# Kernel tuning notes

Measured on AMD Instinct MI355X. Metric: run time of the kernel, lower is better.

The kernel has to match this reference:

```python
import jax, jax.numpy as jnp
import numpy as np

B, NF, L, DEPTH = 128, 1781, 2048, 4
DI, DS, DC, DTR = 8, 32, 4, 1  # d_inner=expand*d_model, d_state, d_conv, dt_rank


def setup_inputs() -> dict:
    key = jax.random.key(0)
    ks = jax.random.split(key, 32)
    n = lambda k, s, sc=0.02: jax.random.normal(k, s, jnp.float32) * sc
    inp = {
        'x': jax.random.normal(ks[0], (B, NF), jnp.float32),
        # projection1: ReLU -> Linear(NF,2048) -> LayerNorm(2048)
        'p1_W': n(ks[1], (L, NF)), 'p1_b': jnp.zeros((L,), jnp.float32),
        'ln1_g': jnp.ones((L,), jnp.float32), 'ln1_b': jnp.zeros((L,), jnp.float32),
        # per-block Mamba params stacked over depth
        'in_W': n(ks[2], (DEPTH, 2 * DI, 1)),
        'conv_w': n(ks[3], (DEPTH, DI, 1, DC), 0.2),
        'conv_b': jnp.zeros((DEPTH, DI), jnp.float32),
        'xp_W': n(ks[4], (DEPTH, DTR + 2 * DS, DI)),
        'dt_W': n(ks[5], (DEPTH, DI, DTR), 0.5),
        'dt_b': n(ks[6], (DEPTH, DI), 0.5) - 4.0,
        'A_log': jnp.log(jnp.tile(jnp.arange(1, DS + 1, dtype=jnp.float32), (DEPTH, DI, 1))),
        'Dp': jnp.ones((DEPTH, DI), jnp.float32),
        'out_W': n(ks[7], (DEPTH, 1, DI)),
        'rms_w': jnp.ones((DEPTH, 1), jnp.float32),
        # projection2: Linear(2048,512) -> LayerNorm(512) -> ReLU -> Linear(512,256)
        'p2a_W': n(ks[8], (512, L)), 'p2a_b': jnp.zeros((512,), jnp.float32),
        'ln2_g': jnp.ones((512,), jnp.float32), 'ln2_b': jnp.zeros((512,), jnp.float32),
        'p2b_W': n(ks[9], (256, 512)), 'p2b_b': jnp.zeros((256,), jnp.float32),
    }
    return inp


def _layernorm(x, g, b, eps=1e-5):
    m = x.mean(-1, keepdims=True)
    v = ((x - m) ** 2).mean(-1, keepdims=True)
    return (x - m) * jax.lax.rsqrt(v + eps) * g + b


def _silu(x):
    return x * jax.nn.sigmoid(x)


def _mamba(x, in_W, conv_w, conv_b, xp_W, dt_W, dt_b, A_log, Dp, out_W):
    # x: (B, L, 1)
    xz = x @ in_W.T                      # (B, L, 2*DI)
    xc, z = jnp.split(xz, 2, axis=-1)    # (B, L, DI) each
    # causal depthwise conv over L
    xt = jnp.transpose(xc, (0, 2, 1))    # (B, DI, L)
    xt = jax.lax.conv_general_dilated(xt, conv_w, (1,), [(DC - 1, 0)],
                                      dimension_numbers=('NCH', 'OIH', 'NCH'),
                                      feature_group_count=DI)
    xc = _silu(jnp.transpose(xt, (0, 2, 1)) + conv_b)   # (B, L, DI)
    x_dbl = xc @ xp_W.T                                  # (B, L, DTR+2*DS)
    dt, Bm, Cm = jnp.split(x_dbl, [DTR, DTR + DS], axis=-1)
    dt = jax.nn.softplus(dt @ dt_W.T + dt_b)             # (B, L, DI)
    A = -jnp.exp(A_log)                                  # (DI, DS)
    dA = jnp.exp(dt[..., None] * A)                      # (B, L, DI, DS)
    dBx = dt[..., None] * Bm[:, :, None, :] * xc[..., None]
    def comb(e1, e2):
        a1, b1 = e1
        a2, b2 = e2
        return (a2 * a1, a2 * b1 + b2)
    _, h = jax.lax.associative_scan(comb, (dA, dBx), axis=1)  # h: (B,L,DI,DS)
    y = jnp.einsum('blds,bls->bld', h, Cm) + Dp * xc
    y = y * _silu(z)
    return y @ out_W.T                                   # (B, L, 1)


def reference(x, p1_W, p1_b, ln1_g, ln1_b, in_W, conv_w, conv_b, xp_W, dt_W, dt_b,
              A_log, Dp, out_W, rms_w, p2a_W, p2a_b, ln2_g, ln2_b, p2b_W, p2b_b):
    h = jax.nn.relu(x) @ p1_W.T + p1_b
    h = _layernorm(h, ln1_g, ln1_b)
    h = h[..., None]                      # (B, L, 1)
    for i in range(DEPTH):
        # RMSNorm over last dim (size 1): mean(x^2) == x^2
        rn = h * jax.lax.rsqrt(h * h + 1e-5) * rms_w[i]
        h = _mamba(rn, in_W[i], conv_w[i], conv_b[i], xp_W[i], dt_W[i], dt_b[i],
                   A_log[i], Dp[i], out_W[i]) + h
    h = h[..., 0]
    h2 = h @ p2a_W.T + p2a_b
    h2 = jax.nn.relu(_layernorm(h2, ln2_g, ln2_b))
    return h2 @ p2b_W.T + p2b_b
```

## Files before the change

### kernel.cpp

```cpp
#include <hip/hip_runtime.h>
#include <math.h>

#define B_    128
#define NF_   1781
#define L_    2048
#define DEPTH_ 4
#define DI_   8
#define DS_   32
#define NXD_  65
#define NC_   32
#define CL_   64
#define MCL_  64
#define KS1_  8
#define KS3_  8
#define LOG2E_ 1.44269504088896f

__device__ __forceinline__ float silu_f(float x) {
    return x / (1.f + __expf(-x));
}
__device__ __forceinline__ float softplus_f(float x) {
    return fmaxf(x, 0.f) + __logf(1.f + __expf(-fabsf(x)));
}
__device__ __forceinline__ float exp2_fast(float x) {
#if __has_builtin(__builtin_amdgcn_exp2f)
    return __builtin_amdgcn_exp2f(x);
#else
    return __expf(x * 0.6931471805599453f);
#endif
}

#define DPP_ADD(x, ctrl)                                                      \
    (x) += __int_as_float(__builtin_amdgcn_update_dpp(                        \
        0, __float_as_int(x), (ctrl), 0xf, 0xf, true))

__device__ __forceinline__ float dpp_sum32_tail(float x) {
    DPP_ADD(x, 0x111);
    DPP_ADD(x, 0x112);
    DPP_ADD(x, 0x114);
    DPP_ADD(x, 0x118);
    DPP_ADD(x, 0x142);
    return x;
}

__device__ __forceinline__ float wave_sum64(float v) {
    v += __shfl_xor(v, 32); v += __shfl_xor(v, 16); v += __shfl_xor(v, 8);
    v += __shfl_xor(v, 4);  v += __shfl_xor(v, 2);  v += __shfl_xor(v, 1);
    return v;
}

__device__ __forceinline__ float block_sum256(float v, float* red) {
    v = wave_sum64(v);
    int tid = threadIdx.x;
    __syncthreads();
    if ((tid & 63) == 0) red[tid >> 6] = v;
    __syncthreads();
    return red[0] + red[1] + red[2] + red[3];
}

__global__ __launch_bounds__(256) void kZero(float4* __restrict__ p) {
    p[blockIdx.x * 256 + threadIdx.x] = make_float4(0.f, 0.f, 0.f, 0.f);
}

__global__ __launch_bounds__(256) void k1_gemm(const float* __restrict__ x,
                                               const float* __restrict__ W,
                                               float* __restrict__ g1) {
    __shared__ float As[32][20];
    __shared__ float Bs[32][65];
    const int n0 = blockIdx.x * 64, m0 = blockIdx.y * 16;
    const int kb = blockIdx.z * 224;
    const int tid = threadIdx.x;
    const int tn = tid & 63, tm = tid >> 6;
    float acc[4] = {0.f, 0.f, 0.f, 0.f};
#pragma unroll 1
    for (int t = 0; t < 7; ++t) {
        const int k0 = kb + t * 32;
#pragma unroll
        for (int j = 0; j < 2; ++j) {
            int idx = tid + 256 * j, k = idx & 31, m = idx >> 5;
            int kk = k0 + k;
            float v = (kk < NF_) ? x[(m0 + m) * NF_ + kk] : 0.f;
            As[k][m] = fmaxf(v, 0.f);
        }
#pragma unroll
        for (int j = 0; j < 8; ++j) {
            int idx = tid + 256 * j, k = idx & 31, n = idx >> 5;
            int kk = k0 + k;
            Bs[k][n] = (kk < NF_) ? W[(size_t)(n0 + n) * NF_ + kk] : 0.f;
        }
        __syncthreads();
#pragma unroll
        for (int k = 0; k < 32; ++k) {
            float4 a = *(const float4*)&As[k][tm * 4];
            float b0 = Bs[k][tn];
            acc[0] = fmaf(a.x, b0, acc[0]);
            acc[1] = fmaf(a.y, b0, acc[1]);
            acc[2] = fmaf(a.z, b0, acc[2]);
            acc[3] = fmaf(a.w, b0, acc[3]);
        }
        __syncthreads();
    }
#pragma unroll
    for (int r = 0; r < 4; ++r)
        atomicAdd(&g1[(m0 + tm * 4 + r) * L_ + n0 + tn], acc[r]);
}

__global__ __launch_bounds__(256) void kLN(float* __restrict__ hg,
                                           const float* __restrict__ bias,
                                           const float* __restrict__ g,
                                           const float* __restrict__ bt) {
    __shared__ float red[4];
    const int tid = threadIdx.x;
    float* h = hg + blockIdx.x * L_;
    float s = 0.f;
    for (int l = tid; l < L_; l += 256) s += h[l] + bias[l];
    s = block_sum256(s, red);
    const float mean = s * (1.f / (float)L_);
    float vs = 0.f;
    for (int l = tid; l < L_; l += 256) {
        float d = h[l] + bias[l] - mean; vs += d * d;
    }
    vs = block_sum256(vs, red);
    const float rstd = rsqrtf(vs * (1.f / (float)L_) + 1e-5f);
    for (int l = tid; l < L_; l += 256)
        h[l] = (h[l] + bias[l] - mean) * rstd * g[l] + bt[l];
}

#define PHASE_LOAD(NEED_ALL)                                                   \
    {                                                                          \
        const float rmsw = rms_w[dep];                                         \
        if (tid < CL_ + 3) {                                                   \
            int lg = c0 - 3 + tid;                                             \
            float hv = (lg >= 0) ? hg[(size_t)b * L_ + lg] : 0.f;              \
            rnb[tid] = (lg >= 0) ? hv * rsqrtf(hv * hv + 1e-5f) * rmsw : 0.f;  \
        }                                                                      \
        int t2 = tid - (CL_ + 3);                                              \
        if (t2 >= 0 && t2 < 32)       Pp[t2]      = conv_w[dep * 32 + t2];     \
        else if (t2 >= 32 && t2 < 40) Pp[t2]      = conv_b[dep * 8 + t2 - 32]; \
        else if (t2 >= 40 && t2 < 56) Pp[t2]      = in_W[dep * 16 + t2 - 40];  \
        else if (t2 >= 56 && t2 < 64) Pp[t2]      = dt_W[dep * 8 + t2 - 56];   \
        else if (t2 >= 64 && t2 < 72) Pp[t2]      = dt_b[dep * 8 + t2 - 64];   \
        else if (NEED_ALL && t2 >= 72 && t2 < 80) Pp[t2] = Dp[dep * 8 + t2 - 72]; \
        else if (NEED_ALL && t2 >= 80 && t2 < 88) Pp[t2] = out_W[dep * 8 + t2 - 80]; \
    }                                                                          \
    __syncthreads();

#define PHASE_CONV()                                                           \
    {                                                                          \
        const int dd = tid & 7, lb = tid >> 3;                                 \
        const float cw0 = Pp[dd * 4], cw1 = Pp[dd * 4 + 1];                    \
        const float cw2 = Pp[dd * 4 + 2], cw3 = Pp[dd * 4 + 3];                \
        const float inw = Pp[40 + dd], cb = Pp[32 + dd];                       \
        const float xp0d = xp_W[dep * (NXD_ * 8) + dd];                        \
        _Pragma("unroll")                                                      \
        for (int jj = 0; jj < CL_ / 32; ++jj) {                                \
            int l = lb + 32 * jj;                                              \
            float sc = cw0 * rnb[l] + cw1 * rnb[l + 1] +                       \
                       cw2 * rnb[l + 2] + cw3 * rnb[l + 3];                    \
            float v = silu_f(inw * sc + cb);                                   \
            xcvb[l * 12 + dd] = v;                                             \
            float p = v * xp0d;                                                \
            DPP_ADD(p, 0x111); DPP_ADD(p, 0x112); DPP_ADD(p, 0x114);          \
            if (dd == 7) dtrawS[l] = p;                                        \
        }                                                                      \
    }                                                                          \
    __syncthreads();

#define PHASE_DT()                                                             \
    {                                                                          \
        const int dd = tid & 7, lb = tid >> 3;                                 \
        const float dtw = Pp[56 + dd], dtb = Pp[64 + dd];                      \
        _Pragma("unroll")                                                      \
        for (int jj = 0; jj < CL_ / 32; ++jj) {                                \
            int l = lb + 32 * jj;                                              \
            float dt = softplus_f(dtrawS[l] * dtw + dtb);                      \
            dtuS[l * 8 + dd] = make_float2(dt * LOG2E_,                        \
                                           dt * xcvb[l * 12 + dd]);            \
        }                                                                      \
    }

__global__ __launch_bounds__(256) void kA(int dep,
    const float* __restrict__ hg, float2* __restrict__ PS,
    const float* __restrict__ in_W,  const float* __restrict__ conv_w,
    const float* __restrict__ conv_b,const float* __restrict__ xp_W,
    const float* __restrict__ dt_W,  const float* __restrict__ dt_b,
    const float* __restrict__ A_log, const float* __restrict__ Dp,
    const float* __restrict__ out_W, const float* __restrict__ rms_w) {
    __shared__ float rnb[CL_ + 3];
    __shared__ float Pp[88];
    __shared__ float xcvb[CL_ * 12];
    __shared__ float dtrawS[CL_];
    __shared__ float BmS[CL_ * 32];
    __shared__ float2 dtuS[CL_ * 8];
    const int c = blockIdx.x, b = blockIdx.y, tid = threadIdx.x;
    const int c0 = c * CL_;

    PHASE_LOAD(0)
    PHASE_CONV()
    {
        const int wave = tid >> 6, lane = tid & 63;
        const int k = lane & 31, half = lane >> 5;
        const float4* wp = (const float4*)(xp_W + dep * (NXD_ * 8) + (k + 1) * 8);
        const float4 wa = wp[0], wb = wp[1];
#pragma unroll
        for (int i = 0; i < CL_ / 8; ++i) {
            int l = wave * (CL_ / 4) + half * (CL_ / 8) + i;
            float4 xa = *(const float4*)&xcvb[l * 12];
            float4 xb = *(const float4*)&xcvb[l * 12 + 4];
            float dot = xa.x * wa.x + xa.y * wa.y + xa.z * wa.z + xa.w * wa.w +
                        xb.x * wb.x + xb.y * wb.y + xb.z * wb.z + xb.w * wb.w;
            BmS[l * 32 + k] = dot;
        }
    }
    PHASE_DT()
    __syncthreads();
    {
        const int d = tid >> 5, s = tid & 31;
        const float Ath = -__expf(A_log[(dep * 8 + d) * 32 + s]);
        float hloc = 0.f, cp = 1.f;
#pragma unroll 4
        for (int l = 0; l < CL_; ++l) {
            float2 du = dtuS[l * 8 + d];
            float dA = exp2_fast(du.x * Ath);
            cp *= dA;
            hloc = fmaf(dA, hloc, du.y * BmS[l * 32 + s]);
        }
        PS[((b * NC_ + c) << 8) + tid] = make_float2(cp, hloc);
    }
}

__global__ __launch_bounds__(256) void kB(const float2* __restrict__ PS,
                                          float* __restrict__ hin) {
    const int b = blockIdx.x, tid = threadIdx.x;
    float h = 0.f;
    for (int c = 0; c < NC_; ++c) {
        hin[((b * NC_ + c) << 8) + tid] = h;
        float2 ps = PS[((b * NC_ + c) << 8) + tid];
        h = fmaf(ps.x, h, ps.y);
    }
}

__global__ __launch_bounds__(256) void kC(int dep,
    float* __restrict__ hg, const float* __restrict__ hin,
    const float* __restrict__ in_W,  const float* __restrict__ conv_w,
    const float* __restrict__ conv_b,const float* __restrict__ xp_W,
    const float* __restrict__ dt_W,  const float* __restrict__ dt_b,
    const float* __restrict__ A_log, const float* __restrict__ Dp,
    const float* __restrict__ out_W, const float* __restrict__ rms_w) {
    __shared__ float rnb[CL_ + 3];
    __shared__ float Pp[88];
    __shared__ float xcvb[CL_ * 12];
    __shared__ float dtrawS[CL_];
    __shared__ float2 BmCmS[CL_ * 32];
    __shared__ float2 dtuS[CL_ * 8];
    __shared__ float ypartS[CL_ * 9];
    __shared__ float offS[CL_];
    const int c = blockIdx.x, b = blockIdx.y, tid = threadIdx.x;
    const int c0 = c * CL_;

    float hst = hin[((b * NC_ + c) << 8) + tid];

    PHASE_LOAD(1)
    PHASE_CONV()
    {
        const int wave = tid >> 6, lane = tid & 63;
        const int k = lane & 31, half = lane >> 5;
        const float4* wp = (const float4*)(xp_W + dep * (NXD_ * 8) + (lane + 1) * 8);
        const float4 wa = wp[0], wb = wp[1];
        float* bc = (float*)BmCmS;
#pragma unroll
        for (int i = 0; i < CL_ / 4; ++i) {
            int l = wave * (CL_ / 4) + i;
            float4 xa = *(const float4*)&xcvb[l * 12];
            float4 xb = *(const float4*)&xcvb[l * 12 + 4];
            float dot = xa.x * wa.x + xa.y * wa.y + xa.z * wa.z + xa.w * wa.w +
                        xb.x * wb.x + xb.y * wb.y + xb.z * wb.z + xb.w * wb.w;
            bc[(l * 32 + k) * 2 + half] = dot;
        }
    }
    PHASE_DT()
    if (tid < CL_) {
        const int l = tid;
        const float rv = rnb[3 + l];
        float o = 0.f;
#pragma unroll
        for (int d2 = 0; d2 < 8; ++d2) {
            float wz = silu_f(rv * Pp[48 + d2]) * Pp[80 + d2];
            o += wz * Pp[72 + d2] * xcvb[l * 12 + d2];
        }
        offS[l] = o;
    }
    __syncthreads();
    {
        const int d = tid >> 5, s = tid & 31;
        const float Ath = -__expf(A_log[(dep * 8 + d) * 32 + s]);
        for (int l0 = 0; l0 < CL_; l0 += 4) {
            float cr[4];
#pragma unroll
            for (int q = 0; q < 4; ++q) {
                int l = l0 + q;
                float2 du = dtuS[l * 8 + d];
                float2 bc = BmCmS[l * 32 + s];
                float dA = exp2_fast(du.x * Ath);
                hst = fmaf(dA, hst, du.y * bc.x);
                cr[q] = hst * bc.y;
            }
#pragma unroll
            for (int q = 0; q < 4; ++q) cr[q] = dpp_sum32_tail(cr[q]);
            if ((tid & 31) == 31) {
#pragma unroll
                for (int q = 0; q < 4; ++q) ypartS[(l0 + q) * 9 + d] = cr[q];
            }
        }
    }
    __syncthreads();
    if (tid < CL_) {
        const int l = tid;
        const float rv = rnb[3 + l];
        float o = offS[l];
#pragma unroll
        for (int d2 = 0; d2 < 8; ++d2) {
            float wz = silu_f(rv * Pp[48 + d2]) * Pp[80 + d2];
            o += wz * ypartS[l * 9 + d2];
        }
        hg[(size_t)b * L_ + c0 + l] += o;
    }
}

__global__ __launch_bounds__(256) void k3_gemm(const float* __restrict__ h,
                                               const float* __restrict__ W,
                                               float* __restrict__ part) {
    __shared__ float As[32][20];
    __shared__ float Bs[32][65];
    const int n0 = blockIdx.x * 64, m0 = blockIdx.y * 16;
    const int kb = blockIdx.z * 256;
    const int tid = threadIdx.x;
    const int tn = tid & 63, tm = tid >> 6;
    float acc[4] = {0.f, 0.f, 0.f, 0.f};
#pragma unroll 1
    for (int t = 0; t < 8; ++t) {
        const int k0 = kb + t * 32;
#pragma unroll
        for (int j = 0; j < 2; ++j) {
            int idx = tid + 256 * j, k = idx & 31, m = idx >> 5;
            As[k][m] = h[(m0 + m) * L_ + k0 + k];
        }
#pragma unroll
        for (int j = 0; j < 8; ++j) {
            int idx = tid + 256 * j, k = idx & 31, n = idx >> 5;
            Bs[k][n] = W[(size_t)(n0 + n) * L_ + k0 + k];
        }
        __syncthreads();
#pragma unroll
        for (int k = 0; k < 32; ++k) {
            float4 a = *(const float4*)&As[k][tm * 4];
            float b0 = Bs[k][tn];
            acc[0] = fmaf(a.x, b0, acc[0]);
            acc[1] = fmaf(a.y, b0, acc[1]);
            acc[2] = fmaf(a.z, b0, acc[2]);
            acc[3] = fmaf(a.w, b0, acc[3]);
        }
        __syncthreads();
    }
    float* pp = part + (size_t)blockIdx.z * (B_ * 512);
#pragma unroll
    for (int r = 0; r < 4; ++r)
        pp[(m0 + tm * 4 + r) * 512 + n0 + tn] = acc[r];
}

__global__ __launch_bounds__(256) void k4_head(const float* __restrict__ part,
    const float* __restrict__ b1,
    const float* __restrict__ g,  const float* __restrict__ bt,
    const float* __restrict__ W2, const float* __restrict__ b2,
    float* __restrict__ out) {
    __shared__ alignas(16) float t2r[512];
    __shared__ alignas(16) float y2[512];
    __shared__ float red[4];
    const int m = blockIdx.x, tid = threadIdx.x;
#pragma unroll
    for (int j = 0; j < 2; ++j) {
        const int n = tid + 256 * j;
        float v = b1[n];
#pragma unroll
        for (int ks = 0; ks < KS3_; ++ks)
            v += part[(size_t)ks * (B_ * 512) + m * 512 + n];
        t2r[n] = v;
    }
    __syncthreads();
    float v0 = t2r[tid], v1 = t2r[tid + 256];
    float s = block_sum256(v0 + v1, red);
    float mean = s * (1.f / 512.f);
    float d0 = v0 - mean, d1 = v1 - mean;
    float var = block_sum256(d0 * d0 + d1 * d1, red) * (1.f / 512.f);
    float rs = rsqrtf(var + 1e-5f);
    y2[tid]       = fmaxf(d0 * rs * g[tid] + bt[tid], 0.f);
    y2[tid + 256] = fmaxf(d1 * rs * g[tid + 256] + bt[tid + 256], 0.f);
    __syncthreads();
    float acc = b2[tid];
    const float* wr = W2 + tid * 512;
    for (int j = 0; j < 512; j += 4) {
        float4 w4 = *(const float4*)&wr[j];
        float4 yv = *(const float4*)&y2[j];
        acc = fmaf(w4.x, yv.x, acc); acc = fmaf(w4.y, yv.y, acc);
        acc = fmaf(w4.z, yv.z, acc); acc = fmaf(w4.w, yv.w, acc);
    }
    out[m * 256 + tid] = acc;
}

struct MambaLds {
    float P_in[16], P_cw[32], P_cb[8], P_dtw[8], P_dtb[8], P_dp[8], P_ow[8];
    alignas(16) float P_xp[NXD_ * 8];
    float rnb[L_ + 3];
    alignas(16) float xcvb[MCL_ * 8];
    alignas(16) float BmS[MCL_ * 33];
    alignas(16) float CmS[MCL_ * 33];
    float2 dtuS[MCL_ * 8];
    float dtrawS[MCL_], offS[MCL_];
    float ypartS[MCL_ * 8];
    float red[4];
};

__device__ void head_body(const float* hrow, float* t2r, float* y2, float* red,
    const float* __restrict__ W1, const float* __restrict__ b1,
    const float* __restrict__ g,  const float* __restrict__ bt,
    const float* __restrict__ W2, const float* __restrict__ b2,
    float* __restrict__ outrow) {
    const int tid = threadIdx.x, wave = tid >> 6, lane = tid & 63;
    for (int i = 0; i < 128; ++i) {
        const int n = wave * 128 + i;
        const float* wr = W1 + (size_t)n * L_;
        float acc = 0.f;
        for (int k0 = lane * 4; k0 < L_; k0 += 256) {
            float4 w4 = *(const float4*)&wr[k0];
            float4 hv = *(const float4*)&hrow[k0];
            acc = fmaf(w4.x, hv.x, acc); acc = fmaf(w4.y, hv.y, acc);
            acc = fmaf(w4.z, hv.z, acc); acc = fmaf(w4.w, hv.w, acc);
        }
        acc = wave_sum64(acc);
        if (lane == 0) t2r[n] = acc + b1[n];
    }
    __syncthreads();
    float v0 = t2r[tid], v1 = t2r[tid + 256];
    float s = block_sum256(v0 + v1, red);
    float mean = s * (1.f / 512.f);
    float d0 = v0 - mean, d1 = v1 - mean;
    float var = block_sum256(d0 * d0 + d1 * d1, red) * (1.f / 512.f);
    float rs = rsqrtf(var + 1e-5f);
    y2[tid]       = fmaxf(d0 * rs * g[tid] + bt[tid], 0.f);
    y2[tid + 256] = fmaxf(d1 * rs * g[tid + 256] + bt[tid + 256], 0.f);
    __syncthreads();
    for (int i = 0; i < 64; ++i) {
        const int n = wave * 64 + i;
        const float* wr = W2 + n * 512;
        float acc = 0.f;
        for (int k0 = lane * 4; k0 < 512; k0 += 256) {
            float4 w4 = *(const float4*)&wr[k0];
            float4 yv = *(const float4*)&y2[k0];
            acc = fmaf(w4.x, yv.x, acc); acc = fmaf(w4.y, yv.y, acc);
            acc = fmaf(w4.z, yv.z, acc); acc = fmaf(w4.w, yv.w, acc);
        }
        acc = wave_sum64(acc);
        if (lane == 0) outrow[n] = acc + b2[n];
    }
}

__device__ void mamba_body(float* h, MambaLds& S,
    const float* __restrict__ ln1_g, const float* __restrict__ ln1_b,
    const float* __restrict__ in_W,  const float* __restrict__ conv_w,
    const float* __restrict__ conv_b,const float* __restrict__ xp_W,
    const float* __restrict__ dt_W,  const float* __restrict__ dt_b,
    const float* __restrict__ A_log, const float* __restrict__ Dp,
    const float* __restrict__ out_W, const float* __restrict__ rms_w) {
    const int tid = threadIdx.x;
    float s = 0.f;
    for (int l = tid; l < L_; l += 256) s += h[l];
    s = block_sum256(s, S.red);
    const float mean = s * (1.f / (float)L_);
    float vs = 0.f;
    for (int l = tid; l < L_; l += 256) { float d = h[l] - mean; vs += d * d; }
    vs = block_sum256(vs, S.red);
    const float rstd = rsqrtf(vs * (1.f / (float)L_) + 1e-5f);
    for (int l = tid; l < L_; l += 256)
        h[l] = (h[l] - mean) * rstd * ln1_g[l] + ln1_b[l];
    __syncthreads();
    const int dd_s = tid >> 5, ss_s = tid & 31;
    for (int dep = 0; dep < DEPTH_; ++dep) {
        if (tid < 16) S.P_in[tid] = in_W[dep * 16 + tid];
        if (tid >= 32 && tid < 64) S.P_cw[tid - 32] = conv_w[dep * 32 + (tid - 32)];
        if (tid >= 64 && tid < 72) S.P_cb[tid - 64] = conv_b[dep * 8 + (tid - 64)];
        if (tid >= 72 && tid < 80) S.P_dtw[tid - 72] = dt_W[dep * 8 + (tid - 72)];
        if (tid >= 80 && tid < 88) S.P_dtb[tid - 80] = dt_b[dep * 8 + (tid - 80)];
        if (tid >= 88 && tid < 96) S.P_dp[tid - 88] = Dp[dep * 8 + (tid - 88)];
        if (tid >= 96 && tid < 104) S.P_ow[tid - 96] = out_W[dep * 8 + (tid - 96)];
        for (int j = tid; j < NXD_ * 8; j += 256) S.P_xp[j] = xp_W[dep * NXD_ * 8 + j];
        const float rmsw = rms_w[dep];
        const float Ath = -__expf(A_log[(dep * 8 + dd_s) * 32 + ss_s]);
        if (tid < 3) S.rnb[tid] = 0.f;
        __syncthreads();
        for (int l = tid; l < L_; l += 256) {
            float hv = h[l];
            S.rnb[3 + l] = hv * rsqrtf(hv * hv + 1e-5f) * rmsw;
        }
        __syncthreads();
        float hst = 0.f;
        for (int c0 = 0; c0 < L_; c0 += MCL_) {
            {
                const int dd = tid & 7, lb = tid >> 3;
                const float cw0 = S.P_cw[dd * 4 + 0], cw1 = S.P_cw[dd * 4 + 1];
                const float cw2 = S.P_cw[dd * 4 + 2], cw3 = S.P_cw[dd * 4 + 3];
                const float inw = S.P_in[dd], cb = S.P_cb[dd];
#pragma unroll
                for (int j = 0; j < MCL_ / 32; ++j) {
                    int l = lb + 32 * j, lg = c0 + l;
                    float sc = cw0 * S.rnb[lg] + cw1 * S.rnb[lg + 1] +
                               cw2 * S.rnb[lg + 2] + cw3 * S.rnb[lg + 3];
                    S.xcvb[l * 8 + dd] = silu_f(inw * sc + cb);
                }
            }
            __syncthreads();
            {
                const int l = tid & 63, q = tid >> 6;
                const float4 xa = *(const float4*)&S.xcvb[l * 8];
                const float4 xb = *(const float4*)&S.xcvb[l * 8 + 4];
                const int j0 = (q == 0) ? 0 : (17 + (q - 1) * 16);
                const int j1 = 17 + q * 16;
                for (int j = j0; j < j1; ++j) {
                    const float4 wa = *(const float4*)&S.P_xp[j * 8];
                    const float4 wb = *(const float4*)&S.P_xp[j * 8 + 4];
                    float dot = xa.x * wa.x + xa.y * wa.y + xa.z * wa.z + xa.w * wa.w +
                                xb.x * wb.x + xb.y * wb.y + xb.z * wb.z + xb.w * wb.w;
                    if (j == 0)      S.dtrawS[l] = dot;
                    else if (j < 33) S.BmS[l * 33 + (j - 1)] = dot;
                    else             S.CmS[l * 33 + (j - 33)] = dot;
                }
            }
            __syncthreads();
            {
                const int dd = tid & 7, lb = tid >> 3;
                const float dtw = S.P_dtw[dd], dtbv = S.P_dtb[dd];
#pragma unroll
                for (int j = 0; j < MCL_ / 32; ++j) {
                    int l = lb + 32 * j;
                    float dt = softplus_f(S.dtrawS[l] * dtw + dtbv);
                    float xcv = S.xcvb[l * 8 + dd];
                    S.dtuS[l * 8 + dd] = make_float2(dt, dt * xcv);
                }
            }
            if (tid < MCL_) {
                const int l = tid;
                const float rv = S.rnb[3 + c0 + l];
                float o = 0.f;
#pragma unroll
                for (int d2 = 0; d2 < 8; ++d2) {
                    float wz = silu_f(rv * S.P_in[8 + d2]) * S.P_ow[d2];
                    o += wz * S.P_dp[d2] * S.xcvb[l * 8 + d2];
                }
                S.offS[l] = o;
            }
            __syncthreads();
#pragma unroll 4
            for (int l = 0; l < MCL_; ++l) {
                float2 du = S.dtuS[l * 8 + dd_s];
                float Bv = S.BmS[l * 33 + ss_s];
                float Cv = S.CmS[l * 33 + ss_s];
                float dA = __expf(du.x * Ath);
                hst = fmaf(dA, hst, du.y * Bv);
                float c = dpp_sum32_tail(hst * Cv);
                if ((tid & 31) == 31) S.ypartS[l * 8 + dd_s] = c;
            }
            __syncthreads();
            if (tid < MCL_) {
                const int l = tid, lg = c0 + l;
                const float rv = S.rnb[3 + lg];
                float o = S.offS[l];
#pragma unroll
                for (int d2 = 0; d2 < 8; ++d2) {
                    float wz = silu_f(rv * S.P_in[8 + d2]) * S.P_ow[d2];
                    o += wz * S.ypartS[l * 8 + d2];
                }
                h[lg] += o;
            }
            __syncthreads();
        }
        __syncthreads();
    }
}

__global__ __launch_bounds__(256) void mega(
    const float* __restrict__ x,
    const float* __restrict__ p1_W, const float* __restrict__ p1_b,
    const float* __restrict__ ln1_g, const float* __restrict__ ln1_b,
    const float* __restrict__ in_W, const float* __restrict__ conv_w,
    const float* __restrict__ conv_b, const float* __restrict__ xp_W,
    const float* __restrict__ dt_W, const float* __restrict__ dt_b,
    const float* __restrict__ A_log, const float* __restrict__ Dp,
    const float* __restrict__ out_W, const float* __restrict__ rms_w,
    const float* __restrict__ p2a_W, const float* __restrict__ p2a_b,
    const float* __restrict__ ln2_g, const float* __restrict__ ln2_b,
    const float* __restrict__ p2b_W, const float* __restrict__ p2b_b,
    float* __restrict__ out) {
    __shared__ alignas(16) float hrow[L_];
    __shared__ MambaLds S;
    const int b = blockIdx.x, tid = threadIdx.x, wave = tid >> 6, lane = tid & 63;
    float* xrow = (float*)S.BmS;
    for (int k = tid; k < 1792; k += 256)
        xrow[k] = (k < NF_) ? fmaxf(x[b * NF_ + k], 0.f) : 0.f;
    __syncthreads();
    for (int i = 0; i < 512; ++i) {
        const int l = wave * 512 + i;
        const float* wr = p1_W + (size_t)l * NF_;
        float acc = 0.f;
        for (int k0 = lane * 4; k0 < NF_; k0 += 256) {
            if (k0 + 3 < NF_) {
                float4 w4 = *(const float4*)&wr[k0];
                float4 xv = *(const float4*)&xrow[k0];
                acc = fmaf(w4.x, xv.x, acc); acc = fmaf(w4.y, xv.y, acc);
                acc = fmaf(w4.z, xv.z, acc); acc = fmaf(w4.w, xv.w, acc);
            } else {
                for (int c = 0; c < 4; ++c)
                    if (k0 + c < NF_) acc = fmaf(wr[k0 + c], xrow[k0 + c], acc);
            }
        }
        acc = wave_sum64(acc);
        if (lane == 0) hrow[l] = acc + p1_b[l];
    }
    __syncthreads();
    mamba_body((float*)hrow, S, ln1_g, ln1_b, in_W, conv_w, conv_b,
               xp_W, dt_W, dt_b, A_log, Dp, out_W, rms_w);
    float* t2r = (float*)S.BmS;
    float* y2  = (float*)S.CmS;
    head_body((const float*)hrow, t2r, y2, S.red, p2a_W, p2a_b,
              ln2_g, ln2_b, p2b_W, p2b_b, out + b * 256);
}

extern "C" void kernel_launch(void* const* d_in, const int* in_sizes, int n_in,
                              void* d_out, int out_size, void* d_ws, size_t ws_size,
                              hipStream_t stream) {
    const float* x     = (const float*)d_in[0];
    const float* p1_W  = (const float*)d_in[1];
    const float* p1_b  = (const float*)d_in[2];
    const float* ln1_g = (const float*)d_in[3];
    const float* ln1_b = (const float*)d_in[4];
    const float* in_W  = (const float*)d_in[5];
    const float* conv_w= (const float*)d_in[6];
    const float* conv_b= (const float*)d_in[7];
    const float* xp_W  = (const float*)d_in[8];
    const float* dt_W  = (const float*)d_in[9];
    const float* dt_b  = (const float*)d_in[10];
    const float* A_log = (const float*)d_in[11];
    const float* Dp    = (const float*)d_in[12];
    const float* out_W = (const float*)d_in[13];
    const float* rms_w = (const float*)d_in[14];
    const float* p2a_W = (const float*)d_in[15];
    const float* p2a_b = (const float*)d_in[16];
    const float* ln2_g = (const float*)d_in[17];
    const float* ln2_b = (const float*)d_in[18];
    const float* p2b_W = (const float*)d_in[19];
    const float* p2b_b = (const float*)d_in[20];
    float* o = (float*)d_out;

    const size_t need = (size_t)B_ * L_ * sizeof(float);
    if (ws_size >= need) {
        float* h = (float*)d_ws;
        float* scr = (float*)d_in[1];
        float2* PS = (float2*)scr;
        float* hin = scr + (size_t)B_ * NC_ * 256 * 2;
        float* t2p = scr;

        kZero<<<L_ * B_ / 1024, 256, 0, stream>>>((float4*)h);
        dim3 grd1(L_ / 64, B_ / 16, KS1_);
        k1_gemm<<<grd1, 256, 0, stream>>>(x, p1_W, h);
        kLN<<<B_, 256, 0, stream>>>(h, p1_b, ln1_g, ln1_b);
        dim3 grdc(NC_, B_);
        for (int dep = 0; dep < DEPTH_; ++dep) {
            kA<<<grdc, 256, 0, stream>>>(dep, h, PS, in_W, conv_w, conv_b,
                                         xp_W, dt_W, dt_b, A_log, Dp, out_W, rms_w);
            kB<<<B_, 256, 0, stream>>>(PS, hin);
            kC<<<grdc, 256, 0, stream>>>(dep, h, hin, in_W, conv_w, conv_b,
                                         xp_W, dt_W, dt_b, A_log, Dp, out_W, rms_w);
        }
        dim3 grd3(512 / 64, B_ / 16, KS3_);
        k3_gemm<<<grd3, 256, 0, stream>>>(h, p2a_W, t2p);
        k4_head<<<B_, 256, 0, stream>>>(t2p, p2a_b, ln2_g, ln2_b,
                                        p2b_W, p2b_b, o);
    } else {
        mega<<<B_, 256, 0, stream>>>(x, p1_W, p1_b, ln1_g, ln1_b, in_W, conv_w,
                                     conv_b, xp_W, dt_W, dt_b, A_log, Dp, out_W,
                                     rms_w, p2a_W, p2a_b, ln2_g, ln2_b,
                                     p2b_W, p2b_b, o);
    }
}
```

Measured before the change: 428.8 us.

## Fold chunk-state prefix scan into kC and enlarge k1 GEMM M tile

```diff
diff --git a/kernel.cpp b/kernel.cpp
--- a/kernel.cpp
+++ b/kernel.cpp
@@ -64,18 +64,18 @@
 __global__ __launch_bounds__(256) void k1_gemm(const float* __restrict__ x,
                                                const float* __restrict__ W,
                                                float* __restrict__ g1) {
-    __shared__ float As[32][20];
+    __shared__ float As[32][36];
     __shared__ float Bs[32][65];
-    const int n0 = blockIdx.x * 64, m0 = blockIdx.y * 16;
+    const int n0 = blockIdx.x * 64, m0 = blockIdx.y * 32;
     const int kb = blockIdx.z * 224;
     const int tid = threadIdx.x;
     const int tn = tid & 63, tm = tid >> 6;
-    float acc[4] = {0.f, 0.f, 0.f, 0.f};
+    float acc[8] = {0.f, 0.f, 0.f, 0.f, 0.f, 0.f, 0.f, 0.f};
 #pragma unroll 1
     for (int t = 0; t < 7; ++t) {
         const int k0 = kb + t * 32;
 #pragma unroll
-        for (int j = 0; j < 2; ++j) {
+        for (int j = 0; j < 4; ++j) {
             int idx = tid + 256 * j, k = idx & 31, m = idx >> 5;
             int kk = k0 + k;
             float v = (kk < NF_) ? x[(m0 + m) * NF_ + kk] : 0.f;
@@ -90,18 +90,19 @@
         __syncthreads();
 #pragma unroll
         for (int k = 0; k < 32; ++k) {
-            float4 a = *(const float4*)&As[k][tm * 4];
+            float4 a0 = *(const float4*)&As[k][tm * 8];
+            float4 a1 = *(const float4*)&As[k][tm * 8 + 4];
             float b0 = Bs[k][tn];
-            acc[0] = fmaf(a.x, b0, acc[0]);
-            acc[1] = fmaf(a.y, b0, acc[1]);
-            acc[2] = fmaf(a.z, b0, acc[2]);
-            acc[3] = fmaf(a.w, b0, acc[3]);
+            acc[0] = fmaf(a0.x, b0, acc[0]); acc[1] = fmaf(a0.y, b0, acc[1]);
+            acc[2] = fmaf(a0.z, b0, acc[2]); acc[3] = fmaf(a0.w, b0, acc[3]);
+            acc[4] = fmaf(a1.x, b0, acc[4]); acc[5] = fmaf(a1.y, b0, acc[5]);
+            acc[6] = fmaf(a1.z, b0, acc[6]); acc[7] = fmaf(a1.w, b0, acc[7]);
         }
         __syncthreads();
     }
 #pragma unroll
-    for (int r = 0; r < 4; ++r)
-        atomicAdd(&g1[(m0 + tm * 4 + r) * L_ + n0 + tn], acc[r]);
+    for (int r = 0; r < 8; ++r)
+        atomicAdd(&g1[(m0 + tm * 8 + r) * L_ + n0 + tn], acc[r]);
 }
 
 __global__ __launch_bounds__(256) void kLN(float* __restrict__ hg,
@@ -228,19 +229,8 @@
     }
 }
 
-__global__ __launch_bounds__(256) void kB(const float2* __restrict__ PS,
-                                          float* __restrict__ hin) {
-    const int b = blockIdx.x, tid = threadIdx.x;
-    float h = 0.f;
-    for (int c = 0; c < NC_; ++c) {
-        hin[((b * NC_ + c) << 8) + tid] = h;
-        float2 ps = PS[((b * NC_ + c) << 8) + tid];
-        h = fmaf(ps.x, h, ps.y);
-    }
-}
-
 __global__ __launch_bounds__(256) void kC(int dep,
-    float* __restrict__ hg, const float* __restrict__ hin,
+    float* __restrict__ hg, const float2* __restrict__ PS,
     const float* __restrict__ in_W,  const float* __restrict__ conv_w,
     const float* __restrict__ conv_b,const float* __restrict__ xp_W,
     const float* __restrict__ dt_W,  const float* __restrict__ dt_b,
@@ -257,7 +247,15 @@
     const int c = blockIdx.x, b = blockIdx.y, tid = threadIdx.x;
     const int c0 = c * CL_;
 
-    float hst = hin[((b * NC_ + c) << 8) + tid];
+    float hin = 0.f;
+    {
+        const float2* psrow = PS + (((size_t)(b * NC_)) << 8) + tid;
+#pragma unroll 4
+        for (int j = 0; j < c; ++j) {
+            float2 ps = psrow[(size_t)j << 8];
+            hin = fmaf(ps.x, hin, ps.y);
+        }
+    }
 
     PHASE_LOAD(1)
     PHASE_CONV()
@@ -293,6 +291,7 @@
     {
         const int d = tid >> 5, s = tid & 31;
         const float Ath = -__expf(A_log[(dep * 8 + d) * 32 + s]);
+        float hst = hin;
         for (int l0 = 0; l0 < CL_; l0 += 4) {
             float cr[4];
 #pragma unroll
@@ -663,19 +662,17 @@
         float* h = (float*)d_ws;
         float* scr = (float*)d_in[1];
         float2* PS = (float2*)scr;
-        float* hin = scr + (size_t)B_ * NC_ * 256 * 2;
         float* t2p = scr;
 
         kZero<<<L_ * B_ / 1024, 256, 0, stream>>>((float4*)h);
-        dim3 grd1(L_ / 64, B_ / 16, KS1_);
+        dim3 grd1(L_ / 64, B_ / 32, KS1_);
         k1_gemm<<<grd1, 256, 0, stream>>>(x, p1_W, h);
         kLN<<<B_, 256, 0, stream>>>(h, p1_b, ln1_g, ln1_b);
         dim3 grdc(NC_, B_);
         for (int dep = 0; dep < DEPTH_; ++dep) {
             kA<<<grdc, 256, 0, stream>>>(dep, h, PS, in_W, conv_w, conv_b,
                                          xp_W, dt_W, dt_b, A_log, Dp, out_W, rms_w);
-            kB<<<B_, 256, 0, stream>>>(PS, hin);
-            kC<<<grdc, 256, 0, stream>>>(dep, h, hin, in_W, conv_w, conv_b,
+            kC<<<grdc, 256, 0, stream>>>(dep, h, PS, in_W, conv_w, conv_b,
                                          xp_W, dt_W, dt_b, A_log, Dp, out_W, rms_w);
         }
         dim3 grd3(512 / 64, B_ / 16, KS3_);
```

After: 454.3 us. +6.0%, slower.
